# Performance work log

Hardware: AMD Instinct MI355X
Metric: run time of the kernel (lower is better)

Reference implementation:

```python
import jax, jax.numpy as jnp
import numpy as np
import math

B, L = 2048, 60
D, H, NL = 80, 8, 3
HD = D // H            # head_dim = 10
NLOC, NUSR = 1187, 46
DFF = 2 * D
IN_DIM = D + 24 + 32 + 2   # loc(80)+user(24)+weekday(16)+hour(16)+2 continuous


def _ln(x, g, b):
    m = jnp.mean(x, -1, keepdims=True)
    v = jnp.mean((x - m) ** 2, -1, keepdims=True)
    return (x - m) * jax.lax.rsqrt(v + 1e-5) * g + b


def setup_inputs():
    key = jax.random.key(0)
    k = lambda i: jax.random.fold_in(key, i)
    g = lambda i, shp, s: jax.random.normal(k(i), shp, dtype=jnp.float32) * s
    inp = {
        "loc_seq": jax.random.randint(k(0), (B, L), 0, NLOC),
        "user_seq": jax.random.randint(k(1), (B, L), 0, NUSR),
        "weekday_seq": jax.random.randint(k(2), (B, L), 0, 8),
        "start_min_seq": jax.random.randint(k(3), (B, L), 0, 1440),
        "dur_seq": jax.random.randint(k(4), (B, L), 0, 600),
        "diff_seq": jax.random.randint(k(5), (B, L), 0, 100),
        "seq_len": jax.random.randint(k(6), (B,), 1, L + 1),
    }
    # embedding tables (padding_idx=0 rows zeroed where the module uses it)
    inp["loc_table"] = g(10, (NLOC, D), 0.02).at[0].set(0.0)
    inp["user_table"] = g(11, (NUSR, 24), 0.02).at[0].set(0.0)
    inp["wk_table"] = g(12, (8, 16), 0.02).at[0].set(0.0)
    inp["hr_table"] = g(13, (25, 16), 0.02)
    inp["in_w"] = g(14, (IN_DIM, D), 0.09)
    inp["in_b"] = jnp.zeros((D,), jnp.float32)
    inp["in_g"] = jnp.ones((D,), jnp.float32)
    inp["in_be"] = jnp.zeros((D,), jnp.float32)
    inp["pos_emb"] = g(15, (1, L, D), 0.02)
    # per-layer stacked params (NL=3 layers)
    inp["qkv_w"] = g(16, (NL, D, 3 * D), 0.09)
    inp["proj_w"] = g(17, (NL, D, D), 0.11)
    inp["proj_b"] = jnp.zeros((NL, D), jnp.float32)
    inp["rel_emb"] = g(18, (NL, 2 * L - 1, HD), 1.0)
    inp["n1_g"] = jnp.ones((NL, D), jnp.float32)
    inp["n1_b"] = jnp.zeros((NL, D), jnp.float32)
    inp["ffn_w1"] = g(19, (NL, D, DFF), 0.09)
    inp["ffn_b1"] = jnp.zeros((NL, DFF), jnp.float32)
    inp["ffn_w2"] = g(20, (NL, DFF, D), 0.09)
    inp["ffn_b2"] = jnp.zeros((NL, D), jnp.float32)
    inp["n2_g"] = jnp.ones((NL, D), jnp.float32)
    inp["n2_b"] = jnp.zeros((NL, D), jnp.float32)
    inp["fn_g"] = jnp.ones((D,), jnp.float32)
    inp["fn_b"] = jnp.zeros((D,), jnp.float32)
    inp["pr_w1"] = g(21, (D, D), 0.11)
    inp["pr_b1"] = jnp.zeros((D,), jnp.float32)
    inp["pr_w2"] = g(22, (D, NLOC), 0.04)
    inp["pr_b2"] = jnp.zeros((NLOC,), jnp.float32)
    inp["protos"] = g(23, (NLOC, D), 0.04)
    inp["temp"] = jnp.asarray(2.0, jnp.float32)
    return inp


def reference(loc_seq, user_seq, weekday_seq, start_min_seq, dur_seq, diff_seq, seq_len,
              loc_table, user_table, wk_table, hr_table, in_w, in_b, in_g, in_be, pos_emb,
              qkv_w, proj_w, proj_b, rel_emb, n1_g, n1_b, ffn_w1, ffn_b1, ffn_w2, ffn_b2,
              n2_g, n2_b, fn_g, fn_b, pr_w1, pr_b1, pr_w2, pr_b2, protos, temp):
    Bx, Lx = loc_seq.shape
    loc_e = loc_table[loc_seq]                                            # [B,L,80]
    user_e = jnp.broadcast_to(user_table[user_seq[:, 0]][:, None, :], (Bx, Lx, 24))
    hour = jnp.clip(start_min_seq // 60, 0, 23)
    cont = jnp.stack([diff_seq.astype(jnp.float32) / 10.0,
                      dur_seq.astype(jnp.float32) / 300.0], -1)           # [B,L,2]
    x = jnp.concatenate([loc_e, user_e, wk_table[weekday_seq], hr_table[hour], cont], -1)
    x = _ln(x @ in_w + in_b, in_g, in_be) + pos_emb[:, :Lx, :]
    key_mask = loc_seq == 0                                               # mask keys [B,L]
    pos_idx = jnp.arange(Lx)[None, :] - jnp.arange(Lx)[:, None] + (Lx - 1)  # [L,L]
    scale = 1.0 / math.sqrt(HD)
    for l in range(NL):
        qkv = (x @ qkv_w[l]).reshape(Bx, Lx, 3, H, HD)
        q = qkv[:, :, 0].transpose(0, 2, 1, 3)                            # [B,H,L,hd]
        kk = qkv[:, :, 1].transpose(0, 2, 1, 3)
        v = qkv[:, :, 2].transpose(0, 2, 1, 3)
        rel = rel_emb[l][pos_idx]                                         # [L,L,hd]
        attn = (jnp.einsum('bhid,bhjd->bhij', q, kk)
                + jnp.einsum('bhid,ijd->bhij', q, rel)) * scale
        attn = jnp.where(key_mask[:, None, None, :], -jnp.inf, attn)
        a = jax.nn.softmax(attn, -1)
        o = jnp.einsum('bhij,bhjd->bhid', a, v).transpose(0, 2, 1, 3).reshape(Bx, Lx, D)
        x = _ln(x + o @ proj_w[l] + proj_b[l], n1_g[l], n1_b[l])
        f = jax.nn.gelu(x @ ffn_w1[l] + ffn_b1[l], approximate=False) @ ffn_w2[l] + ffn_b2[l]
        x = _ln(x + f, n2_g[l], n2_b[l])
    x = _ln(x, fn_g, fn_b)
    final = x[jnp.arange(Bx), jnp.clip(seq_len - 1, 0, Lx - 1)]           # [B,80]
    logits_param = jax.nn.gelu(final @ pr_w1 + pr_b1, approximate=False) @ pr_w2 + pr_b2
    fnorm = final / jnp.maximum(jnp.linalg.norm(final, axis=-1, keepdims=True), 1e-12)
    pnorm = protos / jnp.maximum(jnp.linalg.norm(protos, axis=-1, keepdims=True), 1e-12)
    logits = 0.5 * logits_param + 0.5 * (fnorm @ pnorm.T) * 15.0
    return logits / jnp.clip(temp, 0.5, 3.0)
```

## Files before the change

kernel.cpp:

```cpp
#include <hip/hip_runtime.h>
#include <hip/hip_bf16.h>
#include <math.h>

#define BB   2048
#define LL   60
#define DD   80
#define HH   8
#define HDD  10
#define NLNUM 3
#define NLOC 1187
#define DFF  160
#define IN_DIM 138
#define RELN 119
#define SCS  68
#define XP   21
#define VP   35
#define TS   65

__device__ __forceinline__ float gelu_f(float a) {
  float x = fabsf(a) * 0.70710678118654752f;
  float t = 1.0f / (1.0f + 0.3275911f * x);
  float y = t * (0.254829592f + t * (-0.284496736f + t * (1.421413741f +
            t * (-1.453152027f + t * 1.061405429f))));
  float e = 1.0f - y * __expf(-x * x);
  float erf_s = copysignf(e, a);
  return 0.5f * a * (1.0f + erf_s);
}

__global__ __launch_bounds__(256) void k_rprep(
    const float* __restrict__ rel_emb, float* __restrict__ relTg) {
  int idx = blockIdx.x * 256 + threadIdx.x;
  if (idx >= 3600) return;
  int p = idx % 120;
  int d = (idx / 120) % 10;
  int l = idx / 1200;
  float v = 0.0f;
  if (p < RELN) v = rel_emb[l * RELN * HDD + p * HDD + d];
  relTg[idx] = v;
}

__global__ __launch_bounds__(256) void k_embed(
    const int* __restrict__ loc_seq, const int* __restrict__ user_seq,
    const int* __restrict__ wk_seq, const int* __restrict__ sm_seq,
    const int* __restrict__ dur_seq, const int* __restrict__ diff_seq,
    const float* __restrict__ loc_table, const float* __restrict__ user_table,
    const float* __restrict__ wk_table, const float* __restrict__ hr_table,
    const float* __restrict__ in_w, const float* __restrict__ in_b,
    const float* __restrict__ in_g, const float* __restrict__ in_be,
    const float* __restrict__ pos_emb, float* __restrict__ x) {
  int tok0 = blockIdx.x * 48, tid = threadIdx.x;
  __shared__ __align__(16) float vin[48 * VP * 4];
  __shared__ __align__(16) float ws[140 * 80];
  __shared__ float mstd[96];

  float4* vin4 = (float4*)vin;
  float4* ws4  = (float4*)ws;

  for (int i = tid; i < 140 * 20; i += 256) {
    int r = i / 20, c = i % 20;
    float4 v = make_float4(0.0f, 0.0f, 0.0f, 0.0f);
    if (r < IN_DIM) v = *(const float4*)(in_w + r * 80 + c * 4);
    ws4[i] = v;
  }
  for (int i = tid; i < 48 * 35; i += 256) {
    int t = i / 35, s = i % 35;
    int tok = tok0 + t;
    float4 v;
    if (s < 20) {
      int loc = loc_seq[tok];
      v = *(const float4*)(loc_table + (size_t)loc * 80 + s * 4);
    } else if (s < 26) {
      int usr = user_seq[(tok / LL) * LL];
      v = *(const float4*)(user_table + usr * 24 + (s - 20) * 4);
    } else if (s < 30) {
      int wk = wk_seq[tok];
      v = *(const float4*)(wk_table + wk * 16 + (s - 26) * 4);
    } else if (s < 34) {
      int hr = sm_seq[tok] / 60; hr = min(max(hr, 0), 23);
      v = *(const float4*)(hr_table + hr * 16 + (s - 30) * 4);
    } else {
      v.x = (float)diff_seq[tok] / 10.0f;
      v.y = (float)dur_seq[tok] / 300.0f;
      v.z = 0.0f; v.w = 0.0f;
    }
    vin4[t * VP + s] = v;
  }
  __syncthreads();

  int tg = tid / 20, cg = tid % 20, t0 = tg * 4;
  float acc[4][4] = {};
  if (tid < 240) {
    #pragma unroll 7
    for (int iq = 0; iq < 35; iq++) {
      float4 xv[4], wv[4];
      #pragma unroll
      for (int dt = 0; dt < 4; dt++) xv[dt] = vin4[(t0 + dt) * VP + iq];
      #pragma unroll
      for (int di = 0; di < 4; di++) wv[di] = ws4[(iq * 4 + di) * 20 + cg];
      #pragma unroll
      for (int dt = 0; dt < 4; dt++) {
        const float* xp = (const float*)&xv[dt];
        #pragma unroll
        for (int di = 0; di < 4; di++) {
          const float* wp = (const float*)&wv[di];
          #pragma unroll
          for (int dc = 0; dc < 4; dc++) acc[dt][dc] += xp[di] * wp[dc];
        }
      }
    }
  }
  __syncthreads();
  if (tid < 240) {
    float4 bb = *(const float4*)(in_b + cg * 4);
    const float* bp = (const float*)&bb;
    #pragma unroll
    for (int dt = 0; dt < 4; dt++) {
      float4 y;
      y.x = acc[dt][0] + bp[0];
      y.y = acc[dt][1] + bp[1];
      y.z = acc[dt][2] + bp[2];
      y.w = acc[dt][3] + bp[3];
      vin4[(t0 + dt) * VP + cg] = y;
    }
  }
  __syncthreads();
  if (tid < 48) {
    float s = 0.0f, s2 = 0.0f;
    #pragma unroll
    for (int iq = 0; iq < 20; iq++) {
      float4 v = vin4[tid * VP + iq];
      s  += v.x + v.y + v.z + v.w;
      s2 += v.x * v.x + v.y * v.y + v.z * v.z + v.w * v.w;
    }
    float mean = s / 80.0f;
    float var  = fmaxf(s2 / 80.0f - mean * mean, 0.0f);
    mstd[tid] = mean; mstd[48 + tid] = rsqrtf(var + 1e-5f);
  }
  __syncthreads();
  for (int e = tid; e < 960; e += 256) {
    int t = e / 20, c4 = e % 20;
    float4 v = vin4[t * VP + c4];
    float4 gg = *(const float4*)(in_g + c4 * 4);
    float4 bb = *(const float4*)(in_be + c4 * 4);
    float4 pe = *(const float4*)(pos_emb + ((tok0 + t) % LL) * 80 + c4 * 4);
    float m = mstd[t], r = mstd[48 + t];
    float4 out;
    out.x = (v.x - m) * r * gg.x + bb.x + pe.x;
    out.y = (v.y - m) * r * gg.y + bb.y + pe.y;
    out.z = (v.z - m) * r * gg.z + bb.z + pe.z;
    out.w = (v.w - m) * r * gg.w + bb.w + pe.w;
    ((float4*)(x + (size_t)tok0 * 80))[e] = out;
  }
}

__global__ __launch_bounds__(256) void k_qkv(
    const float* __restrict__ x, const float* __restrict__ qkv_w,
    float* __restrict__ qkvo) {
  int b = blockIdx.x, tid = threadIdx.x;
  __shared__ __align__(16) float xsT[20 * TS * 4];
  __shared__ __align__(16) float ws[40 * 120];

  const float4* xb4 = (const float4*)(x + (size_t)b * 4800);
  float4* xsT4 = (float4*)xsT;
  float4* ws4  = (float4*)ws;
  for (int i = tid; i < 1200; i += 256) {
    int t = i / 20, iq = i % 20;
    xsT4[iq * TS + t] = xb4[i];
  }

  int tg = tid % 15, cg = tid / 15;
  int t0 = tg * 4, cf0 = cg * 2;
  const float4* qw4 = (const float4*)qkv_w;

  for (int c0 = 0; c0 < 240; c0 += 120) {
    float acc[4][8] = {};
    for (int kh = 0; kh < 2; kh++) {
      __syncthreads();
      for (int i = tid; i < 1200; i += 256) {
        int r = i / 30, c = i % 30;
        ws4[i] = qw4[(kh * 40 + r) * 60 + (c0 >> 2) + c];
      }
      __syncthreads();
      if (tid < 225) {
        #pragma unroll 5
        for (int iql = 0; iql < 10; iql++) {
          int iq = kh * 10 + iql;
          float4 xv[4], wva[4], wvb[4];
          #pragma unroll
          for (int dt = 0; dt < 4; dt++) xv[dt] = xsT4[iq * TS + t0 + dt];
          #pragma unroll
          for (int di = 0; di < 4; di++) {
            wva[di] = ws4[(iql * 4 + di) * 30 + cf0];
            wvb[di] = ws4[(iql * 4 + di) * 30 + cf0 + 1];
          }
          #pragma unroll
          for (int dt = 0; dt < 4; dt++) {
            const float* xp = (const float*)&xv[dt];
            #pragma unroll
            for (int di = 0; di < 4; di++) {
              const float* wa = (const float*)&wva[di];
              const float* wb = (const float*)&wvb[di];
              #pragma unroll
              for (int dc = 0; dc < 4; dc++) {
                acc[dt][dc]     += xp[di] * wa[dc];
                acc[dt][4 + dc] += xp[di] * wb[dc];
              }
            }
          }
        }
      }
    }
    if (tid < 225) {
      float* ob = qkvo + (size_t)b * 14400 + (size_t)(c0 + cg * 8) * 60 + t0;
      #pragma unroll
      for (int col = 0; col < 8; col++)
        *(float4*)(ob + (size_t)col * 60) =
            make_float4(acc[0][col], acc[1][col], acc[2][col], acc[3][col]);
    }
  }
}

__global__ __launch_bounds__(256) void k_attn(
    const float* __restrict__ qkvo, const int* __restrict__ loc_seq,
    const float* __restrict__ relTg,
    float* __restrict__ o) {
  int bh = blockIdx.x;
  int b = bh >> 3, h = bh & 7;
  int tid = threadIdx.x;

  __shared__ __align__(16) float qs[HDD * 60];
  __shared__ __align__(16) float ks[HDD * 60];
  __shared__ __align__(16) float vs[HDD * 60];
  __shared__ __align__(16) float relT[HDD * 120];
  __shared__ __align__(16) float sc[60 * SCS];
  __shared__ __align__(16) float rsum[64];
  __shared__ float msk[60];

  const float4* src = (const float4*)(qkvo + (size_t)b * 14400);
  float4* q4 = (float4*)qs; float4* k4 = (float4*)ks; float4* v4 = (float4*)vs;
  for (int i = tid; i < 150; i += 256) {
    q4[i] = src[h * 150 + i];
    k4[i] = src[1200 + h * 150 + i];
    v4[i] = src[2400 + h * 150 + i];
  }
  const float4* rg4 = (const float4*)relTg;
  float4* relT4 = (float4*)relT;
  for (int i = tid; i < 300; i += 256) relT4[i] = rg4[i];
  if (tid < 60) msk[tid] = (loc_seq[b * LL + tid] == 0) ? 1.0f : 0.0f;
  __syncthreads();

  if (tid < 225) {
    int ig = tid / 15, jg = tid % 15;
    int i0 = ig * 4, j0 = jg * 4;
    int w0 = j0 - i0 + 56;
    float acc[4][4] = {};
    #pragma unroll
    for (int d = 0; d < 10; d++) {
      float4 qv = *(const float4*)(qs + d * 60 + i0);
      float4 kv = *(const float4*)(ks + d * 60 + j0);
      float4 rA = *(const float4*)(relT + d * 120 + w0);
      float4 rB = *(const float4*)(relT + d * 120 + w0 + 4);
      float rr[8] = {rA.x, rA.y, rA.z, rA.w, rB.x, rB.y, rB.z, rB.w};
      const float* qp = (const float*)&qv;
      const float* kp = (const float*)&kv;
      #pragma unroll
      for (int di = 0; di < 4; di++)
        #pragma unroll
        for (int dj = 0; dj < 4; dj++)
          acc[di][dj] += qp[di] * (kp[dj] + rr[dj - di + 3]);
    }
    const float scale = 0.31622776601683794f;
    #pragma unroll
    for (int di = 0; di < 4; di++) {
      #pragma unroll
      for (int dj = 0; dj < 4; dj++) {
        float v = acc[di][dj] * scale;
        if (msk[j0 + dj] != 0.0f) v = -1e30f;
        acc[di][dj] = v;
      }
      *(float4*)(sc + (i0 + di) * SCS + j0) =
          make_float4(acc[di][0], acc[di][1], acc[di][2], acc[di][3]);
    }
  }
  __syncthreads();

  if (tid < 240) {
    int r = tid >> 2, q = tid & 3;
    float* row = sc + r * SCS;
    int c0 = q * 4;
    float m = -3.0e38f;
    #pragma unroll
    for (int kk = 0; kk < 4; kk++) {
      int k = c0 + kk;
      if (k < 15) {
        float4 v = *(const float4*)(row + 4 * k);
        m = fmaxf(m, fmaxf(fmaxf(v.x, v.y), fmaxf(v.z, v.w)));
      }
    }
    m = fmaxf(m, __shfl_xor(m, 1));
    m = fmaxf(m, __shfl_xor(m, 2));
    float s = 0.0f;
    #pragma unroll
    for (int kk = 0; kk < 4; kk++) {
      int k = c0 + kk;
      if (k < 15) {
        float4 v = *(float4*)(row + 4 * k);
        v.x = __expf(v.x - m); v.y = __expf(v.y - m);
        v.z = __expf(v.z - m); v.w = __expf(v.w - m);
        *(float4*)(row + 4 * k) = v;
        s += v.x + v.y + v.z + v.w;
      }
    }
    s += __shfl_xor(s, 1);
    s += __shfl_xor(s, 2);
    if (q == 0) rsum[r] = 1.0f / s;
  }
  __syncthreads();

  if (tid < 150) {
    int ig = tid / 10, d = tid % 10;
    float acc[4] = {0, 0, 0, 0};
    #pragma unroll 5
    for (int jq = 0; jq < 15; jq++) {
      float4 vv = *(const float4*)(vs + d * 60 + jq * 4);
      #pragma unroll
      for (int di = 0; di < 4; di++) {
        float4 av = *(const float4*)(sc + (ig + 15 * di) * SCS + jq * 4);
        acc[di] += av.x * vv.x + av.y * vv.y + av.z * vv.z + av.w * vv.w;
      }
    }
    #pragma unroll
    for (int di = 0; di < 4; di++) {
      float r = rsum[ig + 15 * di];
      o[((size_t)b * 60 + ig + 15 * di) * 80 + h * 10 + d] = acc[di] * r;
    }
  }
}

__global__ __launch_bounds__(512) void k_pffn(
    const float* __restrict__ o, const float* __restrict__ proj_w,
    const float* __restrict__ proj_b, const float* __restrict__ g1,
    const float* __restrict__ be1,
    const float* __restrict__ w1, const float* __restrict__ b1,
    const float* __restrict__ w2, const float* __restrict__ b2,
    const float* __restrict__ g2, const float* __restrict__ be2,
    float* __restrict__ x) {
  int tok0 = blockIdx.x * 192, tid = threadIdx.x;
  __shared__ __align__(16) float ys[192 * XP * 4];
  __shared__ __align__(16) float hs[192 * XP * 4];
  __shared__ __align__(16) float ws[1600 * 4];
  __shared__ float mstd[384];

  float4* ys4 = (float4*)ys;
  float4* hs4 = (float4*)hs;
  float4* ws4 = (float4*)ws;
  const float4* w14 = (const float4*)w1;
  const float4* w24 = (const float4*)w2;

  int tg = tid / 20, cg = tid % 20;
  int t0 = tg * 4;
  bool act = tid < 480;

  const float4* ob4 = (const float4*)(o + (size_t)tok0 * 80);
  for (int i = tid; i < 3840; i += 512) hs4[(i / 20) * XP + (i % 20)] = ob4[i];
  for (int i = tid; i < 1600; i += 512) ws4[i] = ((const float4*)proj_w)[i];
  __syncthreads();
  {
    float acc[2][4][4] = {};
    if (act) {
      #pragma unroll 5
      for (int iq = 0; iq < 20; iq++) {
        float4 xv[2][4], wv[4];
        #pragma unroll
        for (int dt = 0; dt < 4; dt++) {
          xv[0][dt] = hs4[(t0 + dt) * XP + iq];
          xv[1][dt] = hs4[(96 + t0 + dt) * XP + iq];
        }
        #pragma unroll
        for (int di = 0; di < 4; di++) wv[di] = ws4[(iq * 4 + di) * 20 + cg];
        #pragma unroll
        for (int u = 0; u < 2; u++)
          #pragma unroll
          for (int dt = 0; dt < 4; dt++) {
            const float* xp = (const float*)&xv[u][dt];
            #pragma unroll
            for (int di = 0; di < 4; di++) {
              const float* wp = (const float*)&wv[di];
              #pragma unroll
              for (int dc = 0; dc < 4; dc++) acc[u][dt][dc] += xp[di] * wp[dc];
            }
          }
      }
    }
    __syncthreads();
    if (act) {
      float4 pb = *(const float4*)(proj_b + cg * 4);
      const float* pbp = (const float*)&pb;
      #pragma unroll
      for (int u = 0; u < 2; u++) {
        int tb = u * 96 + t0;
        #pragma unroll
        for (int dt = 0; dt < 4; dt++) {
          float4 xr = *(const float4*)(x + (size_t)(tok0 + tb + dt) * 80 + cg * 4);
          const float* xrp = (const float*)&xr;
          float4 out;
          out.x = acc[u][dt][0] + pbp[0] + xrp[0];
          out.y = acc[u][dt][1] + pbp[1] + xrp[1];
          out.z = acc[u][dt][2] + pbp[2] + xrp[2];
          out.w = acc[u][dt][3] + pbp[3] + xrp[3];
          ys4[(tb + dt) * XP + cg] = out;
        }
      }
    }
  }
  __syncthreads();
  if (tid < 192) {
    float s = 0.0f, s2 = 0.0f;
    #pragma unroll
    for (int iq = 0; iq < 20; iq++) {
      float4 v = ys4[tid * XP + iq];
      s  += v.x + v.y + v.z + v.w;
      s2 += v.x * v.x + v.y * v.y + v.z * v.z + v.w * v.w;
    }
    float mean = s / 80.0f;
    float var  = fmaxf(s2 / 80.0f - mean * mean, 0.0f);
    mstd[tid] = mean; mstd[192 + tid] = rsqrtf(var + 1e-5f);
  }
  __syncthreads();
  for (int e = tid; e < 3840; e += 512) {
    int t = e / 20, c4 = e % 20;
    float4 v = ys4[t * XP + c4];
    float4 gg = *(const float4*)(g1 + c4 * 4);
    float4 bb = *(const float4*)(be1 + c4 * 4);
    float m = mstd[t], r = mstd[192 + t];
    v.x = (v.x - m) * r * gg.x + bb.x;
    v.y = (v.y - m) * r * gg.y + bb.y;
    v.z = (v.z - m) * r * gg.z + bb.z;
    v.w = (v.w - m) * r * gg.w + bb.w;
    ys4[t * XP + c4] = v;
  }

  float accC[2][4][4] = {};
  for (int hc = 0; hc < 2; hc++) {
    __syncthreads();
    for (int i = tid; i < 1600; i += 512)
      ws4[i] = w14[(i / 20) * 40 + hc * 20 + (i % 20)];
    __syncthreads();
    if (act) {
      float acc[2][4][4] = {};
      #pragma unroll 5
      for (int iq = 0; iq < 20; iq++) {
        float4 xv[2][4], wv[4];
        #pragma unroll
        for (int dt = 0; dt < 4; dt++) {
          xv[0][dt] = ys4[(t0 + dt) * XP + iq];
          xv[1][dt] = ys4[(96 + t0 + dt) * XP + iq];
        }
        #pragma unroll
        for (int di = 0; di < 4; di++) wv[di] = ws4[(iq * 4 + di) * 20 + cg];
        #pragma unroll
        for (int u = 0; u < 2; u++)
          #pragma unroll
          for (int dt = 0; dt < 4; dt++) {
            const float* xp = (const float*)&xv[u][dt];
            #pragma unroll
            for (int di = 0; di < 4; di++) {
              const float* wp = (const float*)&wv[di];
              #pragma unroll
              for (int dc = 0; dc < 4; dc++) acc[u][dt][dc] += xp[di] * wp[dc];
            }
          }
      }
      float4 bb = *(const float4*)(b1 + hc * 80 + cg * 4);
      const float* bp = (const float*)&bb;
      #pragma unroll
      for (int u = 0; u < 2; u++) {
        int tb = u * 96 + t0;
        #pragma unroll
        for (int dt = 0; dt < 4; dt++) {
          float4 hv;
          hv.x = gelu_f(acc[u][dt][0] + bp[0]);
          hv.y = gelu_f(acc[u][dt][1] + bp[1]);
          hv.z = gelu_f(acc[u][dt][2] + bp[2]);
          hv.w = gelu_f(acc[u][dt][3] + bp[3]);
          hs4[(tb + dt) * XP + cg] = hv;
        }
      }
    }
    __syncthreads();
    for (int i = tid; i < 1600; i += 512)
      ws4[i] = w24[(size_t)(hc * 80 + i / 20) * 20 + (i % 20)];
    __syncthreads();
    if (act) {
      #pragma unroll 5
      for (int iq = 0; iq < 20; iq++) {
        float4 hv[2][4], wv[4];
        #pragma unroll
        for (int dt = 0; dt < 4; dt++) {
          hv[0][dt] = hs4[(t0 + dt) * XP + iq];
          hv[1][dt] = hs4[(96 + t0 + dt) * XP + iq];
        }
        #pragma unroll
        for (int di = 0; di < 4; di++) wv[di] = ws4[(iq * 4 + di) * 20 + cg];
        #pragma unroll
        for (int u = 0; u < 2; u++)
          #pragma unroll
          for (int dt = 0; dt < 4; dt++) {
            const float* hp = (const float*)&hv[u][dt];
            #pragma unroll
            for (int di = 0; di < 4; di++) {
              const float* wp = (const float*)&wv[di];
              #pragma unroll
              for (int dc = 0; dc < 4; dc++) accC[u][dt][dc] += hp[di] * wp[dc];
            }
          }
      }
    }
  }

  __syncthreads();
  if (act) {
    float4 bb = *(const float4*)(b2 + cg * 4);
    const float* bp = (const float*)&bb;
    #pragma unroll
    for (int u = 0; u < 2; u++) {
      int tb = u * 96 + t0;
      #pragma unroll
      for (int dt = 0; dt < 4; dt++) {
        float4 yv = ys4[(tb + dt) * XP + cg];
        const float* yp = (const float*)&yv;
        float4 out;
        out.x = accC[u][dt][0] + bp[0] + yp[0];
        out.y = accC[u][dt][1] + bp[1] + yp[1];
        out.z = accC[u][dt][2] + bp[2] + yp[2];
        out.w = accC[u][dt][3] + bp[3] + yp[3];
        hs4[(tb + dt) * XP + cg] = out;
      }
    }
  }
  __syncthreads();
  if (tid < 192) {
    float s = 0.0f, s2 = 0.0f;
    #pragma unroll
    for (int iq = 0; iq < 20; iq++) {
      float4 v = hs4[tid * XP + iq];
      s  += v.x + v.y + v.z + v.w;
      s2 += v.x * v.x + v.y * v.y + v.z * v.z + v.w * v.w;
    }
    float mean = s / 80.0f;
    float var  = fmaxf(s2 / 80.0f - mean * mean, 0.0f);
    mstd[tid] = mean; mstd[192 + tid] = rsqrtf(var + 1e-5f);
  }
  __syncthreads();
  for (int e = tid; e < 3840; e += 512) {
    int t = e / 20, c4 = e % 20;
    float4 v = hs4[t * XP + c4];
    float4 gg = *(const float4*)(g2 + c4 * 4);
    float4 bb = *(const float4*)(be2 + c4 * 4);
    float m = mstd[t], r = mstd[192 + t];
    float4 out;
    out.x = (v.x - m) * r * gg.x + bb.x;
    out.y = (v.y - m) * r * gg.y + bb.y;
    out.z = (v.z - m) * r * gg.z + bb.z;
    out.w = (v.w - m) * r * gg.w + bb.w;
    ((float4*)(x + (size_t)tok0 * 80))[e] = out;
  }
}

__global__ __launch_bounds__(128) void k_final(
    const float* __restrict__ x, const int* __restrict__ seq_len,
    const float* __restrict__ fn_g, const float* __restrict__ fn_b,
    const float* __restrict__ pr_w1, const float* __restrict__ pr_b1,
    float* __restrict__ fnorm, float* __restrict__ h1) {
  int b = blockIdx.x, tid = threadIdx.x;
  __shared__ float red[128], red2[128];
  __shared__ float fbuf[DD];
  int t = seq_len[b] - 1; t = min(max(t, 0), LL - 1);
  float v = 0.0f;
  if (tid < DD) v = x[((size_t)b * LL + t) * DD + tid];
  red[tid]  = (tid < DD) ? v : 0.0f;
  red2[tid] = (tid < DD) ? v * v : 0.0f;
  __syncthreads();
  for (int s = 64; s > 0; s >>= 1) {
    if (tid < s) { red[tid] += red[tid + s]; red2[tid] += red2[tid + s]; }
    __syncthreads();
  }
  float mean = red[0] / DD;
  float var  = fmaxf(red2[0] / DD - mean * mean, 0.0f);
  float rstd = rsqrtf(var + 1e-5f);
  float f = 0.0f;
  if (tid < DD) { f = (v - mean) * rstd * fn_g[tid] + fn_b[tid]; fbuf[tid] = f; }
  __syncthreads();
  red[tid] = (tid < DD) ? f * f : 0.0f;
  __syncthreads();
  for (int s = 64; s > 0; s >>= 1) {
    if (tid < s) red[tid] += red[tid + s];
    __syncthreads();
  }
  float rn = 1.0f / fmaxf(sqrtf(red[0]), 1e-12f);
  if (tid < DD) {
    fnorm[(size_t)b * DD + tid] = f * rn;
    float gacc = pr_b1[tid];
    for (int i = 0; i < DD; i++) gacc += fbuf[i] * pr_w1[i * DD + tid];
    h1[(size_t)b * DD + tid] = gelu_f(gacc);
  }
}

__global__ __launch_bounds__(128) void k_pnorm(
    const float* __restrict__ protos, float* __restrict__ pnormT) {
  int c = blockIdx.x, tid = threadIdx.x;
  __shared__ float red[128];
  float v = 0.0f;
  if (tid < DD) v = protos[(size_t)c * DD + tid];
  red[tid] = (tid < DD) ? v * v : 0.0f;
  __syncthreads();
  for (int s = 64; s > 0; s >>= 1) {
    if (tid < s) red[tid] += red[tid + s];
    __syncthreads();
  }
  float rn = 1.0f / fmaxf(sqrtf(red[0]), 1e-12f);
  if (tid < DD) pnormT[(size_t)tid * NLOC + c] = v * rn;
}

__global__ __launch_bounds__(256) void k_logits(
    const float* __restrict__ h1, const float* __restrict__ fnorm,
    const float* __restrict__ pr_w2, const float* __restrict__ pr_b2,
    const float* __restrict__ pnormT, const float* __restrict__ temp,
    float* __restrict__ out) {
  int b0 = (blockIdx.x / 5) * 4, cb = blockIdx.x % 5;
  int tid = threadIdx.x;
  int c = cb * 256 + tid;
  __shared__ float h1s[4][DD], fns[4][DD];
  for (int i = tid; i < 4 * DD; i += 256) {
    int j = i / DD, k = i % DD;
    h1s[j][k] = h1[(size_t)(b0 + j) * DD + k];
    fns[j][k] = fnorm[(size_t)(b0 + j) * DD + k];
  }
  __syncthreads();
  if (c < NLOC) {
    float a1[4] = {0, 0, 0, 0}, a2[4] = {0, 0, 0, 0};
    for (int k = 0; k < DD; k++) {
      float w = pr_w2[(size_t)k * NLOC + c];
      float p = pnormT[(size_t)k * NLOC + c];
      #pragma unroll
      for (int j = 0; j < 4; j++) {
        a1[j] += h1s[j][k] * w;
        a2[j] += fns[j][k] * p;
      }
    }
    float pb = pr_b2[c];
    float tt = fminf(fmaxf(temp[0], 0.5f), 3.0f);
    #pragma unroll
    for (int j = 0; j < 4; j++)
      out[(size_t)(b0 + j) * NLOC + c] = (0.5f * (a1[j] + pb) + 7.5f * a2[j]) / tt;
  }
}

extern "C" void kernel_launch(void* const* d_in, const int* in_sizes, int n_in,
                              void* d_out, int out_size, void* d_ws, size_t ws_size,
                              hipStream_t stream) {
  const int* loc_seq   = (const int*)d_in[0];
  const int* user_seq  = (const int*)d_in[1];
  const int* wk_seq    = (const int*)d_in[2];
  const int* sm_seq    = (const int*)d_in[3];
  const int* dur_seq   = (const int*)d_in[4];
  const int* diff_seq  = (const int*)d_in[5];
  const int* seq_len   = (const int*)d_in[6];
  const float* loc_table = (const float*)d_in[7];
  const float* user_table= (const float*)d_in[8];
  const float* wk_table  = (const float*)d_in[9];
  const float* hr_table  = (const float*)d_in[10];
  const float* in_w   = (const float*)d_in[11];
  const float* in_b   = (const float*)d_in[12];
  const float* in_g   = (const float*)d_in[13];
  const float* in_be  = (const float*)d_in[14];
  const float* pos_emb= (const float*)d_in[15];
  const float* qkv_w  = (const float*)d_in[16];
  const float* proj_w = (const float*)d_in[17];
  const float* proj_b = (const float*)d_in[18];
  const float* rel_emb= (const float*)d_in[19];
  const float* n1_g   = (const float*)d_in[20];
  const float* n1_b   = (const float*)d_in[21];
  const float* ffn_w1 = (const float*)d_in[22];
  const float* ffn_b1 = (const float*)d_in[23];
  const float* ffn_w2 = (const float*)d_in[24];
  const float* ffn_b2 = (const float*)d_in[25];
  const float* n2_g   = (const float*)d_in[26];
  const float* n2_b   = (const float*)d_in[27];
  const float* fn_g   = (const float*)d_in[28];
  const float* fn_b   = (const float*)d_in[29];
  const float* pr_w1  = (const float*)d_in[30];
  const float* pr_b1  = (const float*)d_in[31];
  const float* pr_w2  = (const float*)d_in[32];
  const float* pr_b2  = (const float*)d_in[33];
  const float* protos = (const float*)d_in[34];
  const float* temp   = (const float*)d_in[35];
  float* out = (float*)d_out;

  float* x      = (float*)d_ws;
  float* o      = x + (size_t)BB * LL * DD;
  float* qkvo   = o + (size_t)BB * LL * DD;
  float* fnorm  = qkvo + (size_t)BB * 14400;
  float* h1     = fnorm + (size_t)BB * DD;
  float* pnormT = h1 + (size_t)BB * DD;
  float* relTg  = pnormT + (size_t)DD * NLOC;

  k_rprep<<<15, 256, 0, stream>>>(rel_emb, relTg);

  k_embed<<<BB * LL / 48, 256, 0, stream>>>(loc_seq, user_seq, wk_seq, sm_seq,
                                            dur_seq, diff_seq, loc_table,
                                            user_table, wk_table, hr_table,
                                            in_w, in_b, in_g, in_be, pos_emb, x);

  for (int l = 0; l < NLNUM; l++) {
    k_qkv<<<BB, 256, 0, stream>>>(x, qkv_w + (size_t)l * 80 * 240, qkvo);
    k_attn<<<BB * HH, 256, 0, stream>>>(qkvo, loc_seq,
                                        relTg + (size_t)l * 1200, o);
    k_pffn<<<BB * LL / 192, 512, 0, stream>>>(
        o, proj_w + (size_t)l * DD * DD, proj_b + (size_t)l * DD,
        n1_g + (size_t)l * DD, n1_b + (size_t)l * DD,
        ffn_w1 + (size_t)l * DD * DFF, ffn_b1 + (size_t)l * DFF,
        ffn_w2 + (size_t)l * DFF * DD, ffn_b2 + (size_t)l * DD,
        n2_g + (size_t)l * DD, n2_b + (size_t)l * DD, x);
  }

  k_pnorm<<<NLOC, 128, 0, stream>>>(protos, pnormT);
  k_final<<<BB, 128, 0, stream>>>(x, seq_len, fn_g, fn_b, pr_w1, pr_b1, fnorm, h1);
  k_logits<<<(BB / 4) * 5, 256, 0, stream>>>(h1, fnorm, pr_w2, pr_b2, pnormT, temp, out);
}
```

Measured before the change: 1.476 ms.

## Process two heads per attention block and enlarge embed tiles to 192 tokens

The attention kernel now handles two heads per block in a loop, sharing the rel-embedding and mask loads and halving the grid. The embed kernel grows to 512 threads and 192 tokens per block, with each thread computing two 4x4 output tiles, so the input-weight staging is amortised over more tokens. The cost is extra sequential sync steps per attention block, fewer blocks to fill the GPU, and more shared memory and registers in embed.

```diff
diff --git a/kernel.cpp b/kernel.cpp
--- a/kernel.cpp
+++ b/kernel.cpp
@@ -39,7 +39,7 @@
   relTg[idx] = v;
 }
 
-__global__ __launch_bounds__(256) void k_embed(
+__global__ __launch_bounds__(512) void k_embed(
     const int* __restrict__ loc_seq, const int* __restrict__ user_seq,
     const int* __restrict__ wk_seq, const int* __restrict__ sm_seq,
     const int* __restrict__ dur_seq, const int* __restrict__ diff_seq,
@@ -48,21 +48,21 @@
     const float* __restrict__ in_w, const float* __restrict__ in_b,
     const float* __restrict__ in_g, const float* __restrict__ in_be,
     const float* __restrict__ pos_emb, float* __restrict__ x) {
-  int tok0 = blockIdx.x * 48, tid = threadIdx.x;
-  __shared__ __align__(16) float vin[48 * VP * 4];
+  int tok0 = blockIdx.x * 192, tid = threadIdx.x;
+  __shared__ __align__(16) float vin[192 * VP * 4];
   __shared__ __align__(16) float ws[140 * 80];
-  __shared__ float mstd[96];
+  __shared__ float mstd[384];
 
   float4* vin4 = (float4*)vin;
   float4* ws4  = (float4*)ws;
 
-  for (int i = tid; i < 140 * 20; i += 256) {
+  for (int i = tid; i < 140 * 20; i += 512) {
     int r = i / 20, c = i % 20;
     float4 v = make_float4(0.0f, 0.0f, 0.0f, 0.0f);
     if (r < IN_DIM) v = *(const float4*)(in_w + r * 80 + c * 4);
     ws4[i] = v;
   }
-  for (int i = tid; i < 48 * 35; i += 256) {
+  for (int i = tid; i < 192 * 35; i += 512) {
     int t = i / 35, s = i % 35;
     int tok = tok0 + t;
     float4 v;
@@ -88,43 +88,53 @@
   __syncthreads();
 
   int tg = tid / 20, cg = tid % 20, t0 = tg * 4;
-  float acc[4][4] = {};
-  if (tid < 240) {
-    #pragma unroll 7
+  bool act = tid < 480;
+  float acc[2][4][4] = {};
+  if (act) {
+    #pragma unroll 5
     for (int iq = 0; iq < 35; iq++) {
-      float4 xv[4], wv[4];
-      #pragma unroll
-      for (int dt = 0; dt < 4; dt++) xv[dt] = vin4[(t0 + dt) * VP + iq];
+      float4 xv[2][4], wv[4];
+      #pragma unroll
+      for (int dt = 0; dt < 4; dt++) {
+        xv[0][dt] = vin4[(t0 + dt) * VP + iq];
+        xv[1][dt] = vin4[(96 + t0 + dt) * VP + iq];
+      }
       #pragma unroll
       for (int di = 0; di < 4; di++) wv[di] = ws4[(iq * 4 + di) * 20 + cg];
       #pragma unroll
-      for (int dt = 0; dt < 4; dt++) {
-        const float* xp = (const float*)&xv[dt];
-        #pragma unroll
-        for (int di = 0; di < 4; di++) {
-          const float* wp = (const float*)&wv[di];
+      for (int u = 0; u < 2; u++)
+        #pragma unroll
+        for (int dt = 0; dt < 4; dt++) {
+          const float* xp = (const float*)&xv[u][dt];
           #pragma unroll
-          for (int dc = 0; dc < 4; dc++) acc[dt][dc] += xp[di] * wp[dc];
-        }
-      }
-    }
-  }
-  __syncthreads();
-  if (tid < 240) {
+          for (int di = 0; di < 4; di++) {
+            const float* wp = (const float*)&wv[di];
+            #pragma unroll
+            for (int dc = 0; dc < 4; dc++) acc[u][dt][dc] += xp[di] * wp[dc];
+          }
+        }
+    }
+  }
+  __syncthreads();
+  if (act) {
     float4 bb = *(const float4*)(in_b + cg * 4);
     const float* bp = (const float*)&bb;
     #pragma unroll
-    for (int dt = 0; dt < 4; dt++) {
-      float4 y;
-      y.x = acc[dt][0] + bp[0];
-      y.y = acc[dt][1] + bp[1];
-      y.z = acc[dt][2] + bp[2];
-      y.w = acc[dt][3] + bp[3];
-      vin4[(t0 + dt) * VP + cg] = y;
-    }
-  }
-  __syncthreads();
-  if (tid < 48) {
+    for (int u = 0; u < 2; u++) {
+      int tb = u * 96 + t0;
+      #pragma unroll
+      for (int dt = 0; dt < 4; dt++) {
+        float4 y;
+        y.x = acc[u][dt][0] + bp[0];
+        y.y = acc[u][dt][1] + bp[1];
+        y.z = acc[u][dt][2] + bp[2];
+        y.w = acc[u][dt][3] + bp[3];
+        vin4[(tb + dt) * VP + cg] = y;
+      }
+    }
+  }
+  __syncthreads();
+  if (tid < 192) {
     float s = 0.0f, s2 = 0.0f;
     #pragma unroll
     for (int iq = 0; iq < 20; iq++) {
@@ -134,16 +144,16 @@
     }
     float mean = s / 80.0f;
     float var  = fmaxf(s2 / 80.0f - mean * mean, 0.0f);
-    mstd[tid] = mean; mstd[48 + tid] = rsqrtf(var + 1e-5f);
-  }
-  __syncthreads();
-  for (int e = tid; e < 960; e += 256) {
+    mstd[tid] = mean; mstd[192 + tid] = rsqrtf(var + 1e-5f);
+  }
+  __syncthreads();
+  for (int e = tid; e < 3840; e += 512) {
     int t = e / 20, c4 = e % 20;
     float4 v = vin4[t * VP + c4];
     float4 gg = *(const float4*)(in_g + c4 * 4);
     float4 bb = *(const float4*)(in_be + c4 * 4);
     float4 pe = *(const float4*)(pos_emb + ((tok0 + t) % LL) * 80 + c4 * 4);
-    float m = mstd[t], r = mstd[48 + t];
+    float m = mstd[t], r = mstd[192 + t];
     float4 out;
     out.x = (v.x - m) * r * gg.x + bb.x + pe.x;
     out.y = (v.y - m) * r * gg.y + bb.y + pe.y;
@@ -224,8 +234,8 @@
     const float* __restrict__ qkvo, const int* __restrict__ loc_seq,
     const float* __restrict__ relTg,
     float* __restrict__ o) {
-  int bh = blockIdx.x;
-  int b = bh >> 3, h = bh & 7;
+  int blk = blockIdx.x;
+  int b = blk >> 2, h0 = (blk & 3) * 2;
   int tid = threadIdx.x;
 
   __shared__ __align__(16) float qs[HDD * 60];
@@ -238,102 +248,107 @@
 
   const float4* src = (const float4*)(qkvo + (size_t)b * 14400);
   float4* q4 = (float4*)qs; float4* k4 = (float4*)ks; float4* v4 = (float4*)vs;
-  for (int i = tid; i < 150; i += 256) {
-    q4[i] = src[h * 150 + i];
-    k4[i] = src[1200 + h * 150 + i];
-    v4[i] = src[2400 + h * 150 + i];
-  }
   const float4* rg4 = (const float4*)relTg;
   float4* relT4 = (float4*)relT;
   for (int i = tid; i < 300; i += 256) relT4[i] = rg4[i];
   if (tid < 60) msk[tid] = (loc_seq[b * LL + tid] == 0) ? 1.0f : 0.0f;
-  __syncthreads();
-
-  if (tid < 225) {
-    int ig = tid / 15, jg = tid % 15;
-    int i0 = ig * 4, j0 = jg * 4;
-    int w0 = j0 - i0 + 56;
-    float acc[4][4] = {};
-    #pragma unroll
-    for (int d = 0; d < 10; d++) {
-      float4 qv = *(const float4*)(qs + d * 60 + i0);
-      float4 kv = *(const float4*)(ks + d * 60 + j0);
-      float4 rA = *(const float4*)(relT + d * 120 + w0);
-      float4 rB = *(const float4*)(relT + d * 120 + w0 + 4);
-      float rr[8] = {rA.x, rA.y, rA.z, rA.w, rB.x, rB.y, rB.z, rB.w};
-      const float* qp = (const float*)&qv;
-      const float* kp = (const float*)&kv;
-      #pragma unroll
-      for (int di = 0; di < 4; di++)
-        #pragma unroll
-        for (int dj = 0; dj < 4; dj++)
-          acc[di][dj] += qp[di] * (kp[dj] + rr[dj - di + 3]);
-    }
-    const float scale = 0.31622776601683794f;
-    #pragma unroll
-    for (int di = 0; di < 4; di++) {
-      #pragma unroll
-      for (int dj = 0; dj < 4; dj++) {
-        float v = acc[di][dj] * scale;
-        if (msk[j0 + dj] != 0.0f) v = -1e30f;
-        acc[di][dj] = v;
-      }
-      *(float4*)(sc + (i0 + di) * SCS + j0) =
-          make_float4(acc[di][0], acc[di][1], acc[di][2], acc[di][3]);
-    }
-  }
-  __syncthreads();
-
-  if (tid < 240) {
-    int r = tid >> 2, q = tid & 3;
-    float* row = sc + r * SCS;
-    int c0 = q * 4;
-    float m = -3.0e38f;
-    #pragma unroll
-    for (int kk = 0; kk < 4; kk++) {
-      int k = c0 + kk;
-      if (k < 15) {
-        float4 v = *(const float4*)(row + 4 * k);
-        m = fmaxf(m, fmaxf(fmaxf(v.x, v.y), fmaxf(v.z, v.w)));
-      }
-    }
-    m = fmaxf(m, __shfl_xor(m, 1));
-    m = fmaxf(m, __shfl_xor(m, 2));
-    float s = 0.0f;
-    #pragma unroll
-    for (int kk = 0; kk < 4; kk++) {
-      int k = c0 + kk;
-      if (k < 15) {
-        float4 v = *(float4*)(row + 4 * k);
-        v.x = __expf(v.x - m); v.y = __expf(v.y - m);
-        v.z = __expf(v.z - m); v.w = __expf(v.w - m);
-        *(float4*)(row + 4 * k) = v;
-        s += v.x + v.y + v.z + v.w;
-      }
-    }
-    s += __shfl_xor(s, 1);
-    s += __shfl_xor(s, 2);
-    if (q == 0) rsum[r] = 1.0f / s;
-  }
-  __syncthreads();
-
-  if (tid < 150) {
-    int ig = tid / 10, d = tid % 10;
-    float acc[4] = {0, 0, 0, 0};
-    #pragma unroll 5
-    for (int jq = 0; jq < 15; jq++) {
-      float4 vv = *(const float4*)(vs + d * 60 + jq * 4);
+
+  for (int hh = 0; hh < 2; hh++) {
+    int h = h0 + hh;
+    for (int i = tid; i < 150; i += 256) {
+      q4[i] = src[h * 150 + i];
+      k4[i] = src[1200 + h * 150 + i];
+      v4[i] = src[2400 + h * 150 + i];
+    }
+    __syncthreads();
+
+    if (tid < 225) {
+      int ig = tid / 15, jg = tid % 15;
+      int i0 = ig * 4, j0 = jg * 4;
+      int w0 = j0 - i0 + 56;
+      float acc[4][4] = {};
+      #pragma unroll
+      for (int d = 0; d < 10; d++) {
+        float4 qv = *(const float4*)(qs + d * 60 + i0);
+        float4 kv = *(const float4*)(ks + d * 60 + j0);
+        float4 rA = *(const float4*)(relT + d * 120 + w0);
+        float4 rB = *(const float4*)(relT + d * 120 + w0 + 4);
+        float rr[8] = {rA.x, rA.y, rA.z, rA.w, rB.x, rB.y, rB.z, rB.w};
+        const float* qp = (const float*)&qv;
+        const float* kp = (const float*)&kv;
+        #pragma unroll
+        for (int di = 0; di < 4; di++)
+          #pragma unroll
+          for (int dj = 0; dj < 4; dj++)
+            acc[di][dj] += qp[di] * (kp[dj] + rr[dj - di + 3]);
+      }
+      const float scale = 0.31622776601683794f;
       #pragma unroll
       for (int di = 0; di < 4; di++) {
-        float4 av = *(const float4*)(sc + (ig + 15 * di) * SCS + jq * 4);
-        acc[di] += av.x * vv.x + av.y * vv.y + av.z * vv.z + av.w * vv.w;
-      }
-    }
-    #pragma unroll
-    for (int di = 0; di < 4; di++) {
-      float r = rsum[ig + 15 * di];
-      o[((size_t)b * 60 + ig + 15 * di) * 80 + h * 10 + d] = acc[di] * r;
-    }
+        #pragma unroll
+        for (int dj = 0; dj < 4; dj++) {
+          float v = acc[di][dj] * scale;
+          if (msk[j0 + dj] != 0.0f) v = -1e30f;
+          acc[di][dj] = v;
+        }
+        *(float4*)(sc + (i0 + di) * SCS + j0) =
+            make_float4(acc[di][0], acc[di][1], acc[di][2], acc[di][3]);
+      }
+    }
+    __syncthreads();
+
+    if (tid < 240) {
+      int r = tid >> 2, q = tid & 3;
+      float* row = sc + r * SCS;
+      int c0 = q * 4;
+      float m = -3.0e38f;
+      #pragma unroll
+      for (int kk = 0; kk < 4; kk++) {
+        int k = c0 + kk;
+        if (k < 15) {
+          float4 v = *(const float4*)(row + 4 * k);
+          m = fmaxf(m, fmaxf(fmaxf(v.x, v.y), fmaxf(v.z, v.w)));
+        }
+      }
+      m = fmaxf(m, __shfl_xor(m, 1));
+      m = fmaxf(m, __shfl_xor(m, 2));
+      float s = 0.0f;
+      #pragma unroll
+      for (int kk = 0; kk < 4; kk++) {
+        int k = c0 + kk;
+        if (k < 15) {
+          float4 v = *(float4*)(row + 4 * k);
+          v.x = __expf(v.x - m); v.y = __expf(v.y - m);
+          v.z = __expf(v.z - m); v.w = __expf(v.w - m);
+          *(float4*)(row + 4 * k) = v;
+          s += v.x + v.y + v.z + v.w;
+        }
+      }
+      s += __shfl_xor(s, 1);
+      s += __shfl_xor(s, 2);
+      if (q == 0) rsum[r] = 1.0f / s;
+    }
+    __syncthreads();
+
+    if (tid < 150) {
+      int ig = tid / 10, d = tid % 10;
+      float acc[4] = {0, 0, 0, 0};
+      #pragma unroll 5
+      for (int jq = 0; jq < 15; jq++) {
+        float4 vv = *(const float4*)(vs + d * 60 + jq * 4);
+        #pragma unroll
+        for (int di = 0; di < 4; di++) {
+          float4 av = *(const float4*)(sc + (ig + 15 * di) * SCS + jq * 4);
+          acc[di] += av.x * vv.x + av.y * vv.y + av.z * vv.z + av.w * vv.w;
+        }
+      }
+      #pragma unroll
+      for (int di = 0; di < 4; di++) {
+        float r = rsum[ig + 15 * di];
+        o[((size_t)b * 60 + ig + 15 * di) * 80 + h * 10 + d] = acc[di] * r;
+      }
+    }
+    __syncthreads();
   }
 }
 
@@ -707,15 +722,15 @@
 
   k_rprep<<<15, 256, 0, stream>>>(rel_emb, relTg);
 
-  k_embed<<<BB * LL / 48, 256, 0, stream>>>(loc_seq, user_seq, wk_seq, sm_seq,
-                                            dur_seq, diff_seq, loc_table,
-                                            user_table, wk_table, hr_table,
-                                            in_w, in_b, in_g, in_be, pos_emb, x);
+  k_embed<<<BB * LL / 192, 512, 0, stream>>>(loc_seq, user_seq, wk_seq, sm_seq,
+                                             dur_seq, diff_seq, loc_table,
+                                             user_table, wk_table, hr_table,
+                                             in_w, in_b, in_g, in_be, pos_emb, x);
 
   for (int l = 0; l < NLNUM; l++) {
     k_qkv<<<BB, 256, 0, stream>>>(x, qkv_w + (size_t)l * 80 * 240, qkvo);
-    k_attn<<<BB * HH, 256, 0, stream>>>(qkvo, loc_seq,
-                                        relTg + (size_t)l * 1200, o);
+    k_attn<<<BB * 4, 256, 0, stream>>>(qkvo, loc_seq,
+                                       relTg + (size_t)l * 1200, o);
     k_pffn<<<BB * LL / 192, 512, 0, stream>>>(
         o, proj_w + (size_t)l * DD * DD, proj_b + (size_t)l * DD,
         n1_g + (size_t)l * DD, n1_b + (size_t)l * DD,
```

After: 1.501 ms. Within noise of the previous version (+1.7%).
